# Optimization experiments

Hardware: AMD Instinct MI355X
Metric: run time of the kernel (lower is better)

## Reference

```python
import jax, jax.numpy as jnp
import numpy as np

S_CENTROIDS = 512
RADIUS = 0.5
NSAMPLE = 32
BN_EPS = 1e-5


def farthest_point_sample(xyz, s):
    # xyz: [B, N, 3] -> idx [B, s], deterministic start at index 0
    B, N, _ = xyz.shape

    def step(carry, _):
        dist, far = carry  # dist [B,N], far [B]
        centroid = jnp.take_along_axis(xyz, far[:, None, None], axis=1)  # [B,1,3]
        d = jnp.sum((xyz - centroid) ** 2, axis=-1)  # [B,N]
        dist = jnp.minimum(dist, d)
        nxt = jnp.argmax(dist, axis=-1).astype(jnp.int32)
        return (dist, nxt), far

    init = (jnp.full((B, N), 1e10, dtype=xyz.dtype), jnp.zeros((B,), jnp.int32))
    _, idx = jax.lax.scan(step, init, None, length=s)
    return idx.T  # [B, s]


def query_ball_point(radius, nsample, xyz, new_xyz):
    # xyz [B,N,3], new_xyz [B,S,3] -> group idx [B,S,nsample]
    B, N, _ = xyz.shape
    sqr = jnp.sum((new_xyz[:, :, None, :] - xyz[:, None, :, :]) ** 2, axis=-1)  # [B,S,N]
    gidx = jnp.where(sqr > radius * radius, N, jnp.arange(N, dtype=jnp.int32)[None, None, :])
    gidx = jnp.sort(gidx, axis=-1)[:, :, :nsample]  # closest-index-first valid ids
    first = gidx[:, :, :1]
    gidx = jnp.where(gidx == N, first, gidx)  # pad misses with first neighbor
    return gidx


def bn_relu(h, gamma, beta):
    # training-mode BatchNorm1d over (batch, length) dims of [BS, C, k]
    m = jnp.mean(h, axis=(0, 2), keepdims=True)
    v = jnp.var(h, axis=(0, 2), keepdims=True)
    hn = (h - m) / jnp.sqrt(v + BN_EPS)
    return jax.nn.relu(hn * gamma[None, :, None] + beta[None, :, None])


def setup_inputs() -> dict:
    key = jax.random.key(0)
    k1, k2, k3, k4 = jax.random.split(key, 4)
    B, N, Din, Dout = 16, 2048, 64, 128  # in_channels=2*Din=128
    x = jax.random.normal(k1, (B, Din, N), dtype=jnp.float32)
    coords = jax.random.uniform(k2, (B, N, 3), dtype=jnp.float32, minval=-1.0, maxval=1.0)
    W1 = jax.random.normal(k3, (Dout, 2 * Din), dtype=jnp.float32) * 0.05  # conv1 1x1 kernel
    W2 = jax.random.normal(k4, (Dout, Dout), dtype=jnp.float32) * 0.05    # conv2 1x1 kernel
    gamma1 = jnp.ones((Dout,), jnp.float32); beta1 = jnp.zeros((Dout,), jnp.float32)
    gamma2 = jnp.ones((Dout,), jnp.float32); beta2 = jnp.zeros((Dout,), jnp.float32)
    return {"x": x, "coords": coords, "W1": W1, "W2": W2,
            "gamma1": gamma1, "beta1": beta1, "gamma2": gamma2, "beta2": beta2}


def reference(x, coords, W1, W2, gamma1, beta1, gamma2, beta2):
    B = x.shape[0]
    feats = jnp.transpose(x, (0, 2, 1))  # [B, N, D]

    fidx = farthest_point_sample(coords, S_CENTROIDS)  # [B, s]
    bidx = jnp.arange(B)[:, None]
    new_xyz = coords[bidx, fidx]        # [B, s, 3]
    new_feat = feats[bidx, fidx]        # [B, s, D]

    gidx = query_ball_point(RADIUS, NSAMPLE, coords, new_xyz)  # [B, s, k]
    grouped = feats[jnp.arange(B)[:, None, None], gidx]        # [B, s, k, D]

    center = new_feat[:, :, None, :]
    agg = jnp.concatenate([grouped - center,
                           jnp.broadcast_to(center, grouped.shape)], axis=-1)  # [B, s, k, 2D]

    b, s, k, d = agg.shape
    h = jnp.transpose(agg, (0, 1, 3, 2)).reshape(b * s, d, k)  # [BS, 2D, k]
    h = bn_relu(jnp.einsum('bck,oc->bok', h, W1), gamma1, beta1)
    h = bn_relu(jnp.einsum('bck,oc->bok', h, W2), gamma2, beta2)
    pooled = jnp.max(h, axis=-1)                  # [BS, out]
    new_feature = jnp.transpose(pooled.reshape(b, s, -1), (0, 2, 1))  # [B, out, s]
    return new_xyz, new_feature
```

## Files before the change

kernel.cpp:

```cpp
#include <hip/hip_runtime.h>
#include <cstdint>

typedef unsigned int uint;
typedef unsigned short ushort_t;
typedef unsigned long long ull;
typedef __attribute__((ext_vector_type(8))) short bf16x8;
typedef __attribute__((ext_vector_type(4))) float f32x4;
typedef __attribute__((ext_vector_type(2))) float f32x2;

#define B_   16
#define N_   2048
#define S_   512
#define G_   8192
#define DIN  64
#define DOUT 128
#define K_   32
#define ATS  136

__device__ __forceinline__ uint bf16b(float f) {
  uint u = __float_as_uint(f);
  return (u + 0x7fffu + ((u >> 16) & 1u)) >> 16;
}
__device__ __forceinline__ float bf2f(uint b) { return __uint_as_float(b << 16); }

template<int CTRL, int RM>
__device__ __forceinline__ ull dpp_max_step(ull x) {
  uint lo = (uint)x, hi = (uint)(x >> 32);
  uint nlo = (uint)__builtin_amdgcn_update_dpp((int)lo, (int)lo, CTRL, RM, 0xf, true);
  uint nhi = (uint)__builtin_amdgcn_update_dpp((int)hi, (int)hi, CTRL, RM, 0xf, true);
  ull y = ((ull)nhi << 32) | (ull)nlo;
  return x > y ? x : y;
}

__global__ __launch_bounds__(256) void front_kernel(const float* __restrict__ coords,
    const float* __restrict__ x, const float* __restrict__ W1,
    const float* __restrict__ W2, int* __restrict__ fidx,
    float* __restrict__ out_xyz, ushort_t* __restrict__ xT,
    ushort_t* __restrict__ Bp1, ushort_t* __restrict__ Bpd,
    ushort_t* __restrict__ Bp2) {
  int blk = blockIdx.x;
  int tid = threadIdx.x;
  if (blk < 16) {
    int b = blk;
    const float* cb = coords + (size_t)b * (N_ * 3);
    __shared__ float sptx[N_], spty[N_], sptz[N_];
    __shared__ ull   skey[2][4];
    __shared__ int   sfar[S_];
    int lane = tid & 63, wid = tid >> 6;
    for (int j = tid; j < N_; j += 256) {
      sptx[j] = cb[3 * j]; spty[j] = cb[3 * j + 1]; sptz[j] = cb[3 * j + 2];
    }
    f32x2 px[4], py[4], pz[4], dist[4];
    uint nidx[8];
    int j0 = tid * 8;
#pragma unroll
    for (int p = 0; p < 4; ++p) {
      int j = j0 + 2 * p;
      px[p].x = cb[3 * j];     py[p].x = cb[3 * j + 1]; pz[p].x = cb[3 * j + 2];
      px[p].y = cb[3 * j + 3]; py[p].y = cb[3 * j + 4]; pz[p].y = cb[3 * j + 5];
      dist[p].x = 1e10f; dist[p].y = 1e10f;
      nidx[2 * p] = ~(uint)j; nidx[2 * p + 1] = ~(uint)(j + 1);
    }
    float cx = cb[0], cy = cb[1], cz = cb[2];
    uint far = 0;
    __syncthreads();
    for (int s = 0; s < S_; ++s) {
      if (tid == 0) sfar[s] = (int)far;
      f32x2 c2x = {cx, cx}, c2y = {cy, cy}, c2z = {cz, cz};
      ull best = 0;
#pragma unroll
      for (int p = 0; p < 4; ++p) {
        f32x2 dx, dy, dz, qx, qy, qz, s1, s2;
        asm("v_pk_add_f32 %0, %1, %2 neg_lo:[0,1] neg_hi:[0,1]" : "=v"(dx) : "v"(px[p]), "v"(c2x));
        asm("v_pk_add_f32 %0, %1, %2 neg_lo:[0,1] neg_hi:[0,1]" : "=v"(dy) : "v"(py[p]), "v"(c2y));
        asm("v_pk_add_f32 %0, %1, %2 neg_lo:[0,1] neg_hi:[0,1]" : "=v"(dz) : "v"(pz[p]), "v"(c2z));
        asm("v_pk_mul_f32 %0, %1, %1" : "=v"(qx) : "v"(dx));
        asm("v_pk_mul_f32 %0, %1, %1" : "=v"(qy) : "v"(dy));
        asm("v_pk_mul_f32 %0, %1, %1" : "=v"(qz) : "v"(dz));
        asm("v_pk_add_f32 %0, %1, %2" : "=v"(s1) : "v"(qx), "v"(qy));
        asm("v_pk_add_f32 %0, %1, %2" : "=v"(s2) : "v"(s1), "v"(qz));
        float n0 = fminf(dist[p].x, s2.x);
        float n1 = fminf(dist[p].y, s2.y);
        dist[p].x = n0; dist[p].y = n1;
        ull p0 = ((ull)__float_as_uint(n0) << 32) | (ull)nidx[2 * p];
        ull p1 = ((ull)__float_as_uint(n1) << 32) | (ull)nidx[2 * p + 1];
        best = best > p0 ? best : p0;
        best = best > p1 ? best : p1;
      }
      best = dpp_max_step<0x111, 0xf>(best);
      best = dpp_max_step<0x112, 0xf>(best);
      best = dpp_max_step<0x114, 0xf>(best);
      best = dpp_max_step<0x118, 0xf>(best);
      best = dpp_max_step<0x142, 0xa>(best);
      best = dpp_max_step<0x143, 0xc>(best);
      int pb = s & 1;
      if (lane == 63) skey[pb][wid] = best;
      __syncthreads();
      ull k0 = skey[pb][0], k1 = skey[pb][1], k2 = skey[pb][2], k3 = skey[pb][3];
      uint w0 = ~(uint)k0, w1 = ~(uint)k1, w2 = ~(uint)k2, w3 = ~(uint)k3;
      float x0 = sptx[w0], y0 = spty[w0], z0 = sptz[w0];
      float x1 = sptx[w1], y1 = spty[w1], z1 = sptz[w1];
      float x2 = sptx[w2], y2 = spty[w2], z2 = sptz[w2];
      float x3 = sptx[w3], y3 = spty[w3], z3 = sptz[w3];
      bool t01 = k0 > k1, t23 = k2 > k3;
      ull ka = t01 ? k0 : k1;  float xa = t01 ? x0 : x1, ya = t01 ? y0 : y1, za = t01 ? z0 : z1;
      ull kb = t23 ? k2 : k3;  float xb = t23 ? x2 : x3, yb = t23 ? y2 : y3, zb = t23 ? z2 : z3;
      bool tw = ka > kb;
      far = ~(uint)(tw ? ka : kb);
      cx = tw ? xa : xb; cy = tw ? ya : yb; cz = tw ? za : zb;
    }
    __syncthreads();
    for (int s2 = tid; s2 < S_; s2 += 256) {
      int f = sfar[s2];
      fidx[b * S_ + s2] = f;
      int o = (b * S_ + s2) * 3;
      out_xyz[o] = sptx[f]; out_xyz[o + 1] = spty[f]; out_xyz[o + 2] = sptz[f];
    }
  } else if (blk < 528) {
    __shared__ float tile[64][65];
    int blk2 = blk - 16;
    int b = blk2 >> 5;
    int n0 = (blk2 & 31) * 64;
    int nn = tid & 63, c4 = tid >> 6;
    const float* xb = x + (size_t)b * (DIN * N_);
#pragma unroll
    for (int i = 0; i < 16; ++i) {
      int c = c4 * 16 + i;
      tile[nn][c] = xb[(size_t)c * N_ + n0 + nn];
    }
    __syncthreads();
#pragma unroll
    for (int i = 0; i < 16; ++i) {
      int n = c4 * 16 + i;
      xT[((size_t)b * N_ + n0 + n) * 64 + nn] = (ushort_t)bf16b(tile[n][nn]);
    }
  } else {
    int i = (blk - 528) * 256 + tid;
    int j2 = i & 7, l = (i >> 3) & 63;
    {
      int kc = (i >> 9) & 3, nt = i >> 11;
      int o2 = nt * 16 + (l & 15);
      int c2 = kc * 32 + ((l >> 4) * 8) + j2;
      Bp2[i] = (ushort_t)bf16b(W2[o2 * 128 + c2]);
    }
    if (i < 8192) {
      int kc = (i >> 9) & 1, nt = (i >> 10) & 7;
      int o2 = nt * 16 + (l & 15);
      int c2 = kc * 32 + ((l >> 4) * 8) + j2;
      float wa = W1[o2 * 128 + c2];
      float wb = W1[o2 * 128 + 64 + c2];
      Bp1[i] = (ushort_t)bf16b(wa);
      Bpd[i] = (ushort_t)bf16b(wb - wa);
    }
  }
}

__global__ __launch_bounds__(256) void gemm1_kernel(const ushort_t* __restrict__ xT,
    const float* __restrict__ coords, const int* __restrict__ fidx,
    const ushort_t* __restrict__ Bp1, const ushort_t* __restrict__ Bpd,
    int* __restrict__ gidx, float* __restrict__ psum, float* __restrict__ psq) {
  __shared__ int sgidx[4][K_];
  int tid = threadIdx.x;
  int lane = tid & 63, wid = tid >> 6;
  int g = __builtin_amdgcn_readfirstlane(blockIdx.x * 4 + wid);
  int b = g >> 9;
  const float* cb = coords + (size_t)b * (N_ * 3);
  int nf = fidx[g];
  {
    float cx = cb[3 * nf], cy = cb[3 * nf + 1], cz = cb[3 * nf + 2];
    int cnt = 0, first = 0;
    bool hasfirst = false;
    for (int base = 0; base < N_; base += 64) {
      int j = base + lane;
      float dx = __fsub_rn(cb[3 * j], cx);
      float dy = __fsub_rn(cb[3 * j + 1], cy);
      float dz = __fsub_rn(cb[3 * j + 2], cz);
      float d = __fadd_rn(__fadd_rn(__fmul_rn(dx, dx), __fmul_rn(dy, dy)), __fmul_rn(dz, dz));
      bool in = (d <= 0.25f);
      ull m = __ballot(in);
      if (in) {
        int pos = cnt + __popcll(m & ((1ull << lane) - 1ull));
        if (pos < K_) sgidx[wid][pos] = j;
      }
      if (!hasfirst && m) { first = base + (__ffsll((long long)m) - 1); hasfirst = true; }
      cnt += __popcll(m);
      if (cnt >= K_) break;
    }
    if (cnt < K_) {
      for (int p = cnt + lane; p < K_; p += 64) sgidx[wid][p] = first;
    }
  }
  if (lane < K_) gidx[g * K_ + lane] = sgidx[wid][lane];
  int l15 = lane & 15, r8 = (lane >> 4) * 8;
  const ushort_t* xb64 = xT + (size_t)b * N_ * 64;
  f32x4 acc[2][8];
#pragma unroll
  for (int nt = 0; nt < 8; ++nt) acc[0][nt] = (f32x4){0.f, 0.f, 0.f, 0.f};
#pragma unroll
  for (int kc = 0; kc < 2; ++kc) {
    bf16x8 cu = *(const bf16x8*)(xb64 + nf * 64 + kc * 32 + r8);
#pragma unroll
    for (int nt = 0; nt < 8; ++nt) {
      bf16x8 bf = *(const bf16x8*)(Bpd + ((nt * 2 + kc) * 64 + lane) * 8);
      acc[0][nt] = __builtin_amdgcn_mfma_f32_16x16x32_bf16(cu, bf, acc[0][nt], 0, 0, 0);
    }
  }
#pragma unroll
  for (int nt = 0; nt < 8; ++nt) acc[1][nt] = acc[0][nt];
  int gi0 = sgidx[wid][l15];
  int gi1 = sgidx[wid][16 + l15];
#pragma unroll
  for (int kc = 0; kc < 2; ++kc) {
    bf16x8 af0 = *(const bf16x8*)(xb64 + (size_t)gi0 * 64 + kc * 32 + r8);
    bf16x8 af1 = *(const bf16x8*)(xb64 + (size_t)gi1 * 64 + kc * 32 + r8);
#pragma unroll
    for (int nt = 0; nt < 8; ++nt) {
      bf16x8 bf = *(const bf16x8*)(Bp1 + ((nt * 2 + kc) * 64 + lane) * 8);
      acc[0][nt] = __builtin_amdgcn_mfma_f32_16x16x32_bf16(af0, bf, acc[0][nt], 0, 0, 0);
      acc[1][nt] = __builtin_amdgcn_mfma_f32_16x16x32_bf16(af1, bf, acc[1][nt], 0, 0, 0);
    }
  }
#pragma unroll
  for (int nt = 0; nt < 8; ++nt) {
    float s = 0.f, q = 0.f;
#pragma unroll
    for (int mt = 0; mt < 2; ++mt)
#pragma unroll
      for (int r = 0; r < 4; ++r) { float a = acc[mt][nt][r]; s += a; q = fmaf(a, a, q); }
    s += __shfl_xor(s, 16, 64); s += __shfl_xor(s, 32, 64);
    q += __shfl_xor(q, 16, 64); q += __shfl_xor(q, 32, 64);
    if (lane < 16) {
      int o = nt * 16 + lane;
      psum[o * G_ + g] = s; psq[o * G_ + g] = q;
    }
  }
}

__global__ __launch_bounds__(256) void bn_finalize(const float* __restrict__ psum,
    const float* __restrict__ psq, const float* __restrict__ gamma,
    const float* __restrict__ beta, float* __restrict__ bnp) {
  int o = blockIdx.x, tid = threadIdx.x;
  double s = 0.0, q = 0.0;
  for (int g = tid; g < G_; g += 256) { s += (double)psum[o * G_ + g]; q += (double)psq[o * G_ + g]; }
  __shared__ double ss[256], qq[256];
  ss[tid] = s; qq[tid] = q; __syncthreads();
  for (int off = 128; off > 0; off >>= 1) {
    if (tid < off) { ss[tid] += ss[tid + off]; qq[tid] += qq[tid + off]; }
    __syncthreads();
  }
  if (tid == 0) {
    double n = 262144.0;
    double mean = ss[0] / n, var = qq[0] / n - mean * mean;
    float scv = (float)((double)gamma[o] / sqrt(var + 1e-5));
    bnp[2 * o] = scv;
    bnp[2 * o + 1] = (float)((double)beta[o] - mean * (double)scv);
  }
}

__global__ __launch_bounds__(256) void gemm2_kernel(const ushort_t* __restrict__ xT,
    const int* __restrict__ fidx, const int* __restrict__ gidx,
    const ushort_t* __restrict__ Bp1, const ushort_t* __restrict__ Bpd,
    const ushort_t* __restrict__ Bp2, const float* __restrict__ bnp1,
    float* __restrict__ psum, float* __restrict__ psq,
    float* __restrict__ hmax, float* __restrict__ hmin) {
  __shared__ ushort_t actT[4][32 * ATS];
  int tid = threadIdx.x;
  int lane = tid & 63, wid = tid >> 6;
  int g = __builtin_amdgcn_readfirstlane(blockIdx.x * 4 + wid);
  int b = g >> 9;
  int l15 = lane & 15, r8 = (lane >> 4) * 8;
  const ushort_t* xb64 = xT + (size_t)b * N_ * 64;
  int nf = fidx[g];
  f32x4 acc[2][8];
#pragma unroll
  for (int nt = 0; nt < 8; ++nt) acc[0][nt] = (f32x4){0.f, 0.f, 0.f, 0.f};
#pragma unroll
  for (int kc = 0; kc < 2; ++kc) {
    bf16x8 cu = *(const bf16x8*)(xb64 + nf * 64 + kc * 32 + r8);
#pragma unroll
    for (int nt = 0; nt < 8; ++nt) {
      bf16x8 bf = *(const bf16x8*)(Bpd + ((nt * 2 + kc) * 64 + lane) * 8);
      acc[0][nt] = __builtin_amdgcn_mfma_f32_16x16x32_bf16(cu, bf, acc[0][nt], 0, 0, 0);
    }
  }
#pragma unroll
  for (int nt = 0; nt < 8; ++nt) acc[1][nt] = acc[0][nt];
  int gi0 = gidx[g * K_ + l15];
  int gi1 = gidx[g * K_ + 16 + l15];
#pragma unroll
  for (int kc = 0; kc < 2; ++kc) {
    bf16x8 af0 = *(const bf16x8*)(xb64 + (size_t)gi0 * 64 + kc * 32 + r8);
    bf16x8 af1 = *(const bf16x8*)(xb64 + (size_t)gi1 * 64 + kc * 32 + r8);
#pragma unroll
    for (int nt = 0; nt < 8; ++nt) {
      bf16x8 bf = *(const bf16x8*)(Bp1 + ((nt * 2 + kc) * 64 + lane) * 8);
      acc[0][nt] = __builtin_amdgcn_mfma_f32_16x16x32_bf16(af0, bf, acc[0][nt], 0, 0, 0);
      acc[1][nt] = __builtin_amdgcn_mfma_f32_16x16x32_bf16(af1, bf, acc[1][nt], 0, 0, 0);
    }
  }
  float s1v[8], t1v[8];
#pragma unroll
  for (int nt = 0; nt < 8; ++nt) {
    int o = nt * 16 + l15;
    s1v[nt] = bnp1[2 * o]; t1v[nt] = bnp1[2 * o + 1];
  }
  ushort_t* aw = actT[wid];
#pragma unroll
  for (int mt = 0; mt < 2; ++mt)
#pragma unroll
    for (int r = 0; r < 4; ++r) {
      int k = mt * 16 + (lane >> 4) * 4 + r;
#pragma unroll
      for (int nt = 0; nt < 8; ++nt) {
        float a = fmaxf(fmaf(acc[mt][nt][r], s1v[nt], t1v[nt]), 0.f);
        aw[k * ATS + nt * 16 + l15] = (ushort_t)bf16b(a);
      }
    }
  f32x4 acc2[2][8];
#pragma unroll
  for (int mt = 0; mt < 2; ++mt)
#pragma unroll
    for (int nt = 0; nt < 8; ++nt) acc2[mt][nt] = (f32x4){0.f, 0.f, 0.f, 0.f};
#pragma unroll
  for (int kc = 0; kc < 4; ++kc) {
    bf16x8 afrag[2];
#pragma unroll
    for (int mt = 0; mt < 2; ++mt)
      afrag[mt] = *(const bf16x8*)(aw + (mt * 16 + l15) * ATS + kc * 32 + r8);
#pragma unroll
    for (int nt = 0; nt < 8; ++nt) {
      bf16x8 bfrag = *(const bf16x8*)(Bp2 + ((nt * 4 + kc) * 64 + lane) * 8);
      acc2[0][nt] = __builtin_amdgcn_mfma_f32_16x16x32_bf16(afrag[0], bfrag, acc2[0][nt], 0, 0, 0);
      acc2[1][nt] = __builtin_amdgcn_mfma_f32_16x16x32_bf16(afrag[1], bfrag, acc2[1][nt], 0, 0, 0);
    }
  }
#pragma unroll
  for (int nt = 0; nt < 8; ++nt) {
    float s = 0.f, q = 0.f, mx = -1e30f, mn = 1e30f;
#pragma unroll
    for (int mt = 0; mt < 2; ++mt)
#pragma unroll
      for (int r = 0; r < 4; ++r) {
        float a = acc2[mt][nt][r];
        s += a; q = fmaf(a, a, q); mx = fmaxf(mx, a); mn = fminf(mn, a);
      }
    s += __shfl_xor(s, 16, 64); s += __shfl_xor(s, 32, 64);
    q += __shfl_xor(q, 16, 64); q += __shfl_xor(q, 32, 64);
    mx = fmaxf(mx, __shfl_xor(mx, 16, 64)); mx = fmaxf(mx, __shfl_xor(mx, 32, 64));
    mn = fminf(mn, __shfl_xor(mn, 16, 64)); mn = fminf(mn, __shfl_xor(mn, 32, 64));
    if (lane < 16) {
      int o = nt * 16 + lane;
      psum[o * G_ + g] = s; psq[o * G_ + g] = q;
      hmax[o * G_ + g] = mx; hmin[o * G_ + g] = mn;
    }
  }
}

__global__ __launch_bounds__(256) void bn2pool_kernel(const float* __restrict__ psum,
    const float* __restrict__ psq, const float* __restrict__ gamma,
    const float* __restrict__ beta, const float* __restrict__ hmax,
    const float* __restrict__ hmin, float* __restrict__ out) {
  int o = blockIdx.x, tid = threadIdx.x;
  double s = 0.0, q = 0.0;
  for (int g = tid; g < G_; g += 256) { s += (double)psum[o * G_ + g]; q += (double)psq[o * G_ + g]; }
  __shared__ double ss[256], qq[256];
  __shared__ float sb[2];
  ss[tid] = s; qq[tid] = q; __syncthreads();
  for (int off = 128; off > 0; off >>= 1) {
    if (tid < off) { ss[tid] += ss[tid + off]; qq[tid] += qq[tid + off]; }
    __syncthreads();
  }
  if (tid == 0) {
    double n = 262144.0;
    double mean = ss[0] / n, var = qq[0] / n - mean * mean;
    float scv = (float)((double)gamma[o] / sqrt(var + 1e-5));
    sb[0] = scv;
    sb[1] = (float)((double)beta[o] - mean * (double)scv);
  }
  __syncthreads();
  float scv = sb[0], tf = sb[1];
  for (int g = tid; g < G_; g += 256) {
    float v = (scv >= 0.f) ? hmax[o * G_ + g] : hmin[o * G_ + g];
    int b = g >> 9, s2 = g & 511;
    out[((b << 7) + o) * 512 + s2] = fmaxf(fmaf(scv, v, tf), 0.f);
  }
}

extern "C" void kernel_launch(void* const* d_in, const int* in_sizes, int n_in,
                              void* d_out, int out_size, void* d_ws, size_t ws_size,
                              hipStream_t stream) {
  const float* x      = (const float*)d_in[0];
  const float* coords = (const float*)d_in[1];
  const float* W1     = (const float*)d_in[2];
  const float* W2     = (const float*)d_in[3];
  const float* gamma1 = (const float*)d_in[4];
  const float* beta1  = (const float*)d_in[5];
  const float* gamma2 = (const float*)d_in[6];
  const float* beta2  = (const float*)d_in[7];
  float* out = (float*)d_out;
  char* ws = (char*)d_ws;
  float* psum1 = (float*)(ws);
  float* psq1  = (float*)(ws + 4194304);
  float* psum2 = (float*)(ws + 8388608);
  float* psq2  = (float*)(ws + 12582912);
  float* hmax  = (float*)(ws + 16777216);
  float* hmin  = (float*)(ws + 20971520);
  ushort_t* xT = (ushort_t*)(ws + 25165824);
  ushort_t* Bp1 = (ushort_t*)(ws + 29360128);
  ushort_t* Bpd = (ushort_t*)(ws + 29376512);
  ushort_t* Bp2 = (ushort_t*)(ws + 29392896);
  float* bnp1  = (float*)(ws + 29425664);
  int* fidx    = (int*)(ws + 29427712);
  int* gidx    = (int*)(ws + 29460480);

  front_kernel<<<592, 256, 0, stream>>>(coords, x, W1, W2, fidx, out, xT, Bp1, Bpd, Bp2);
  gemm1_kernel<<<2048, 256, 0, stream>>>(xT, coords, fidx, Bp1, Bpd, gidx, psum1, psq1);
  bn_finalize<<<128, 256, 0, stream>>>(psum1, psq1, gamma1, beta1, bnp1);
  gemm2_kernel<<<2048, 256, 0, stream>>>(xT, fidx, gidx, Bp1, Bpd, Bp2, bnp1,
                                         psum2, psq2, hmax, hmin);
  bn2pool_kernel<<<128, 256, 0, stream>>>(psum2, psq2, gamma2, beta2, hmax, hmin,
                                          out + 24576);
}
```

Baseline: 350.5 us.

## Run farthest-point sampling in a single wavefront per batch without block barriers

Farthest-point sampling becomes its own kernel with one 64-lane wavefront per batch. Each lane holds 32 points in registers and tracks its local argmax with a float value plus a small index, instead of packing 64-bit keys per point. Each step's result comes from a DPP reduction and a readlane, which removes the per-iteration LDS key exchange and __syncthreads. The x transpose and weight packing move to a separate aux kernel. That adds a launch, and the aux work now runs after FPS instead of overlapping with it in the same grid.

Result: slower. 557.7 us (+59.1%).

```diff
diff --git a/kernel.cpp b/kernel.cpp
--- a/kernel.cpp
+++ b/kernel.cpp
@@ -32,95 +32,81 @@
   return x > y ? x : y;
 }
 
-__global__ __launch_bounds__(256) void front_kernel(const float* __restrict__ coords,
-    const float* __restrict__ x, const float* __restrict__ W1,
-    const float* __restrict__ W2, int* __restrict__ fidx,
-    float* __restrict__ out_xyz, ushort_t* __restrict__ xT,
-    ushort_t* __restrict__ Bp1, ushort_t* __restrict__ Bpd,
-    ushort_t* __restrict__ Bp2) {
+__global__ __launch_bounds__(64, 1) void fps1_kernel(const float* __restrict__ coords,
+                                                     int* __restrict__ fidx,
+                                                     float* __restrict__ out_xyz) {
+  int b = blockIdx.x;
+  int lane = threadIdx.x;
+  const float* cb = coords + (size_t)b * (N_ * 3);
+  __shared__ float sptx[N_], spty[N_], sptz[N_];
+  __shared__ int sfar[S_];
+  f32x2 px[16], py[16], pz[16], dist[16];
+  const float* lb = cb + lane * 96;
+#pragma unroll
+  for (int i = 0; i < 16; ++i) {
+    float4 v4 = *(const float4*)(lb + 6 * i);
+    float2 v2 = *(const float2*)(lb + 6 * i + 4);
+    px[i] = (f32x2){v4.x, v4.w};
+    py[i] = (f32x2){v4.y, v2.x};
+    pz[i] = (f32x2){v4.z, v2.y};
+    dist[i] = (f32x2){1e10f, 1e10f};
+    *(f32x2*)&sptx[lane * 32 + 2 * i] = px[i];
+    *(f32x2*)&spty[lane * 32 + 2 * i] = py[i];
+    *(f32x2*)&sptz[lane * 32 + 2 * i] = pz[i];
+  }
+  float cx = cb[0], cy = cb[1], cz = cb[2];
+  uint far = 0;
+  uint jbase = (uint)lane * 32;
+  for (int s = 0; s < S_; ++s) {
+    if (lane == 0) sfar[s] = (int)far;
+    f32x2 c2x = {cx, cx}, c2y = {cy, cy}, c2z = {cz, cz};
+    float bestv = -1.f; uint bestloc = 0;
+#pragma unroll
+    for (int i = 0; i < 16; ++i) {
+      f32x2 dx, dy, dz, qx, qy, qz, s1, s2;
+      asm("v_pk_add_f32 %0, %1, %2 neg_lo:[0,1] neg_hi:[0,1]" : "=v"(dx) : "v"(px[i]), "v"(c2x));
+      asm("v_pk_add_f32 %0, %1, %2 neg_lo:[0,1] neg_hi:[0,1]" : "=v"(dy) : "v"(py[i]), "v"(c2y));
+      asm("v_pk_add_f32 %0, %1, %2 neg_lo:[0,1] neg_hi:[0,1]" : "=v"(dz) : "v"(pz[i]), "v"(c2z));
+      asm("v_pk_mul_f32 %0, %1, %1" : "=v"(qx) : "v"(dx));
+      asm("v_pk_mul_f32 %0, %1, %1" : "=v"(qy) : "v"(dy));
+      asm("v_pk_mul_f32 %0, %1, %1" : "=v"(qz) : "v"(dz));
+      asm("v_pk_add_f32 %0, %1, %2" : "=v"(s1) : "v"(qx), "v"(qy));
+      asm("v_pk_add_f32 %0, %1, %2" : "=v"(s2) : "v"(s1), "v"(qz));
+      float n0 = fminf(dist[i].x, s2.x);
+      float n1 = fminf(dist[i].y, s2.y);
+      dist[i].x = n0; dist[i].y = n1;
+      bool g0 = n0 > bestv; bestv = g0 ? n0 : bestv; bestloc = g0 ? (uint)(2 * i) : bestloc;
+      bool g1 = n1 > bestv; bestv = g1 ? n1 : bestv; bestloc = g1 ? (uint)(2 * i + 1) : bestloc;
+    }
+    ull best = ((ull)__float_as_uint(bestv) << 32) | (ull)(~(jbase + bestloc));
+    best = dpp_max_step<0x111, 0xf>(best);
+    best = dpp_max_step<0x112, 0xf>(best);
+    best = dpp_max_step<0x114, 0xf>(best);
+    best = dpp_max_step<0x118, 0xf>(best);
+    best = dpp_max_step<0x142, 0xa>(best);
+    best = dpp_max_step<0x143, 0xc>(best);
+    uint klo = (uint)__builtin_amdgcn_readlane((int)(uint)best, 63);
+    far = ~klo;
+    cx = sptx[far]; cy = spty[far]; cz = sptz[far];
+  }
+  for (int s2 = lane; s2 < S_; s2 += 64) {
+    int f = sfar[s2];
+    fidx[b * S_ + s2] = f;
+    int o = (b * S_ + s2) * 3;
+    out_xyz[o] = sptx[f]; out_xyz[o + 1] = spty[f]; out_xyz[o + 2] = sptz[f];
+  }
+}
+
+__global__ __launch_bounds__(256) void aux_kernel(const float* __restrict__ x,
+    const float* __restrict__ W1, const float* __restrict__ W2,
+    ushort_t* __restrict__ xT, ushort_t* __restrict__ Bp1,
+    ushort_t* __restrict__ Bpd, ushort_t* __restrict__ Bp2) {
   int blk = blockIdx.x;
   int tid = threadIdx.x;
-  if (blk < 16) {
-    int b = blk;
-    const float* cb = coords + (size_t)b * (N_ * 3);
-    __shared__ float sptx[N_], spty[N_], sptz[N_];
-    __shared__ ull   skey[2][4];
-    __shared__ int   sfar[S_];
-    int lane = tid & 63, wid = tid >> 6;
-    for (int j = tid; j < N_; j += 256) {
-      sptx[j] = cb[3 * j]; spty[j] = cb[3 * j + 1]; sptz[j] = cb[3 * j + 2];
-    }
-    f32x2 px[4], py[4], pz[4], dist[4];
-    uint nidx[8];
-    int j0 = tid * 8;
-#pragma unroll
-    for (int p = 0; p < 4; ++p) {
-      int j = j0 + 2 * p;
-      px[p].x = cb[3 * j];     py[p].x = cb[3 * j + 1]; pz[p].x = cb[3 * j + 2];
-      px[p].y = cb[3 * j + 3]; py[p].y = cb[3 * j + 4]; pz[p].y = cb[3 * j + 5];
-      dist[p].x = 1e10f; dist[p].y = 1e10f;
-      nidx[2 * p] = ~(uint)j; nidx[2 * p + 1] = ~(uint)(j + 1);
-    }
-    float cx = cb[0], cy = cb[1], cz = cb[2];
-    uint far = 0;
-    __syncthreads();
-    for (int s = 0; s < S_; ++s) {
-      if (tid == 0) sfar[s] = (int)far;
-      f32x2 c2x = {cx, cx}, c2y = {cy, cy}, c2z = {cz, cz};
-      ull best = 0;
-#pragma unroll
-      for (int p = 0; p < 4; ++p) {
-        f32x2 dx, dy, dz, qx, qy, qz, s1, s2;
-        asm("v_pk_add_f32 %0, %1, %2 neg_lo:[0,1] neg_hi:[0,1]" : "=v"(dx) : "v"(px[p]), "v"(c2x));
-        asm("v_pk_add_f32 %0, %1, %2 neg_lo:[0,1] neg_hi:[0,1]" : "=v"(dy) : "v"(py[p]), "v"(c2y));
-        asm("v_pk_add_f32 %0, %1, %2 neg_lo:[0,1] neg_hi:[0,1]" : "=v"(dz) : "v"(pz[p]), "v"(c2z));
-        asm("v_pk_mul_f32 %0, %1, %1" : "=v"(qx) : "v"(dx));
-        asm("v_pk_mul_f32 %0, %1, %1" : "=v"(qy) : "v"(dy));
-        asm("v_pk_mul_f32 %0, %1, %1" : "=v"(qz) : "v"(dz));
-        asm("v_pk_add_f32 %0, %1, %2" : "=v"(s1) : "v"(qx), "v"(qy));
-        asm("v_pk_add_f32 %0, %1, %2" : "=v"(s2) : "v"(s1), "v"(qz));
-        float n0 = fminf(dist[p].x, s2.x);
-        float n1 = fminf(dist[p].y, s2.y);
-        dist[p].x = n0; dist[p].y = n1;
-        ull p0 = ((ull)__float_as_uint(n0) << 32) | (ull)nidx[2 * p];
-        ull p1 = ((ull)__float_as_uint(n1) << 32) | (ull)nidx[2 * p + 1];
-        best = best > p0 ? best : p0;
-        best = best > p1 ? best : p1;
-      }
-      best = dpp_max_step<0x111, 0xf>(best);
-      best = dpp_max_step<0x112, 0xf>(best);
-      best = dpp_max_step<0x114, 0xf>(best);
-      best = dpp_max_step<0x118, 0xf>(best);
-      best = dpp_max_step<0x142, 0xa>(best);
-      best = dpp_max_step<0x143, 0xc>(best);
-      int pb = s & 1;
-      if (lane == 63) skey[pb][wid] = best;
-      __syncthreads();
-      ull k0 = skey[pb][0], k1 = skey[pb][1], k2 = skey[pb][2], k3 = skey[pb][3];
-      uint w0 = ~(uint)k0, w1 = ~(uint)k1, w2 = ~(uint)k2, w3 = ~(uint)k3;
-      float x0 = sptx[w0], y0 = spty[w0], z0 = sptz[w0];
-      float x1 = sptx[w1], y1 = spty[w1], z1 = sptz[w1];
-      float x2 = sptx[w2], y2 = spty[w2], z2 = sptz[w2];
-      float x3 = sptx[w3], y3 = spty[w3], z3 = sptz[w3];
-      bool t01 = k0 > k1, t23 = k2 > k3;
-      ull ka = t01 ? k0 : k1;  float xa = t01 ? x0 : x1, ya = t01 ? y0 : y1, za = t01 ? z0 : z1;
-      ull kb = t23 ? k2 : k3;  float xb = t23 ? x2 : x3, yb = t23 ? y2 : y3, zb = t23 ? z2 : z3;
-      bool tw = ka > kb;
-      far = ~(uint)(tw ? ka : kb);
-      cx = tw ? xa : xb; cy = tw ? ya : yb; cz = tw ? za : zb;
-    }
-    __syncthreads();
-    for (int s2 = tid; s2 < S_; s2 += 256) {
-      int f = sfar[s2];
-      fidx[b * S_ + s2] = f;
-      int o = (b * S_ + s2) * 3;
-      out_xyz[o] = sptx[f]; out_xyz[o + 1] = spty[f]; out_xyz[o + 2] = sptz[f];
-    }
-  } else if (blk < 528) {
+  if (blk < 512) {
     __shared__ float tile[64][65];
-    int blk2 = blk - 16;
-    int b = blk2 >> 5;
-    int n0 = (blk2 & 31) * 64;
+    int b = blk >> 5;
+    int n0 = (blk & 31) * 64;
     int nn = tid & 63, c4 = tid >> 6;
     const float* xb = x + (size_t)b * (DIN * N_);
 #pragma unroll
@@ -135,7 +121,7 @@
       xT[((size_t)b * N_ + n0 + n) * 64 + nn] = (ushort_t)bf16b(tile[n][nn]);
     }
   } else {
-    int i = (blk - 528) * 256 + tid;
+    int i = (blk - 512) * 256 + tid;
     int j2 = i & 7, l = (i >> 3) & 63;
     {
       int kc = (i >> 9) & 3, nt = i >> 11;
@@ -413,7 +399,8 @@
   int* fidx    = (int*)(ws + 29427712);
   int* gidx    = (int*)(ws + 29460480);
 
-  front_kernel<<<592, 256, 0, stream>>>(coords, x, W1, W2, fidx, out, xT, Bp1, Bpd, Bp2);
+  fps1_kernel<<<16, 64, 0, stream>>>(coords, fidx, out);
+  aux_kernel<<<576, 256, 0, stream>>>(x, W1, W2, xT, Bp1, Bpd, Bp2);
   gemm1_kernel<<<2048, 256, 0, stream>>>(xT, coords, fidx, Bp1, Bpd, gidx, psum1, psq1);
   bn_finalize<<<128, 256, 0, stream>>>(psum1, psq1, gamma1, beta1, bnp1);
   gemm2_kernel<<<2048, 256, 0, stream>>>(xT, fidx, gidx, Bp1, Bpd, Bp2, bnp1,
```

## Transpose BN partial-stat layout and split reductions into two-stage kernels

Applied to the files above, without the earlier changes.

The per-group partial sums, squares, max and min are now stored group-major ([G][128]) instead of channel-major. The GEMM epilogue stores become contiguous across the 16 lanes. The BN statistics reduction is split into a 128-block partial pass and a single-block finalize, replacing the per-channel block reductions. Pooling becomes its own kernel that transposes through shared memory for coalesced output writes. This adds two extra kernel launches and a dependency on a single-block kernel.

New measurement: 363.8 us. +3.8%, slower.

```diff
diff --git a/kernel.cpp b/kernel.cpp
--- a/kernel.cpp
+++ b/kernel.cpp
@@ -231,29 +231,51 @@
     q += __shfl_xor(q, 16, 64); q += __shfl_xor(q, 32, 64);
     if (lane < 16) {
       int o = nt * 16 + lane;
-      psum[o * G_ + g] = s; psq[o * G_ + g] = q;
-    }
-  }
-}
-
-__global__ __launch_bounds__(256) void bn_finalize(const float* __restrict__ psum,
-    const float* __restrict__ psq, const float* __restrict__ gamma,
+      psum[(size_t)g * 128 + o] = s; psq[(size_t)g * 128 + o] = q;
+    }
+  }
+}
+
+__global__ __launch_bounds__(256) void bnA_kernel(const float* __restrict__ psum,
+    const float* __restrict__ psq, double* __restrict__ part_s,
+    double* __restrict__ part_q) {
+  int bid = blockIdx.x, tid = threadIdx.x;
+  int o = tid & 127, half = tid >> 7;
+  int g0 = bid * 64;
+  double s = 0.0, q = 0.0;
+  for (int r = half; r < 64; r += 2) {
+    s += (double)psum[(size_t)(g0 + r) * 128 + o];
+    q += (double)psq[(size_t)(g0 + r) * 128 + o];
+  }
+  __shared__ double ds[256], dq[256];
+  ds[tid] = s; dq[tid] = q;
+  __syncthreads();
+  if (tid < 128) {
+    part_s[bid * 128 + tid] = ds[tid] + ds[tid + 128];
+    part_q[bid * 128 + tid] = dq[tid] + dq[tid + 128];
+  }
+}
+
+__global__ __launch_bounds__(256) void bnB_kernel(const double* __restrict__ part_s,
+    const double* __restrict__ part_q, const float* __restrict__ gamma,
     const float* __restrict__ beta, float* __restrict__ bnp) {
-  int o = blockIdx.x, tid = threadIdx.x;
+  int tid = threadIdx.x;
+  int o = tid & 127, half = tid >> 7;
   double s = 0.0, q = 0.0;
-  for (int g = tid; g < G_; g += 256) { s += (double)psum[o * G_ + g]; q += (double)psq[o * G_ + g]; }
-  __shared__ double ss[256], qq[256];
-  ss[tid] = s; qq[tid] = q; __syncthreads();
-  for (int off = 128; off > 0; off >>= 1) {
-    if (tid < off) { ss[tid] += ss[tid + off]; qq[tid] += qq[tid + off]; }
-    __syncthreads();
-  }
-  if (tid == 0) {
+  for (int p = half; p < 128; p += 2) {
+    s += part_s[p * 128 + o];
+    q += part_q[p * 128 + o];
+  }
+  __shared__ double ds[256], dq[256];
+  ds[tid] = s; dq[tid] = q;
+  __syncthreads();
+  if (tid < 128) {
+    double S = ds[tid] + ds[tid + 128], Q = dq[tid] + dq[tid + 128];
     double n = 262144.0;
-    double mean = ss[0] / n, var = qq[0] / n - mean * mean;
-    float scv = (float)((double)gamma[o] / sqrt(var + 1e-5));
-    bnp[2 * o] = scv;
-    bnp[2 * o + 1] = (float)((double)beta[o] - mean * (double)scv);
+    double mean = S / n, var = Q / n - mean * mean;
+    float scv = (float)((double)gamma[tid] / sqrt(var + 1e-5));
+    bnp[2 * tid] = scv;
+    bnp[2 * tid + 1] = (float)((double)beta[tid] - mean * (double)scv);
   }
 }
 
@@ -350,39 +372,35 @@
     mn = fminf(mn, __shfl_xor(mn, 16, 64)); mn = fminf(mn, __shfl_xor(mn, 32, 64));
     if (lane < 16) {
       int o = nt * 16 + lane;
-      psum[o * G_ + g] = s; psq[o * G_ + g] = q;
-      hmax[o * G_ + g] = mx; hmin[o * G_ + g] = mn;
-    }
-  }
-}
-
-__global__ __launch_bounds__(256) void bn2pool_kernel(const float* __restrict__ psum,
-    const float* __restrict__ psq, const float* __restrict__ gamma,
-    const float* __restrict__ beta, const float* __restrict__ hmax,
-    const float* __restrict__ hmin, float* __restrict__ out) {
-  int o = blockIdx.x, tid = threadIdx.x;
-  double s = 0.0, q = 0.0;
-  for (int g = tid; g < G_; g += 256) { s += (double)psum[o * G_ + g]; q += (double)psq[o * G_ + g]; }
-  __shared__ double ss[256], qq[256];
-  __shared__ float sb[2];
-  ss[tid] = s; qq[tid] = q; __syncthreads();
-  for (int off = 128; off > 0; off >>= 1) {
-    if (tid < off) { ss[tid] += ss[tid + off]; qq[tid] += qq[tid + off]; }
-    __syncthreads();
-  }
-  if (tid == 0) {
-    double n = 262144.0;
-    double mean = ss[0] / n, var = qq[0] / n - mean * mean;
-    float scv = (float)((double)gamma[o] / sqrt(var + 1e-5));
-    sb[0] = scv;
-    sb[1] = (float)((double)beta[o] - mean * (double)scv);
+      psum[(size_t)g * 128 + o] = s; psq[(size_t)g * 128 + o] = q;
+      hmax[(size_t)g * 128 + o] = mx; hmin[(size_t)g * 128 + o] = mn;
+    }
+  }
+}
+
+__global__ __launch_bounds__(256) void pool_kernel(const float* __restrict__ hmax,
+    const float* __restrict__ hmin, const float* __restrict__ bnp2,
+    float* __restrict__ out) {
+  __shared__ float hx[16][132], hn[16][132];
+  int bid = blockIdx.x;
+  int g0 = bid * 16;
+  int b = g0 >> 9, s0 = g0 & 511;
+  int tid = threadIdx.x;
+  int col = tid & 127, rp = tid >> 7;
+#pragma unroll
+  for (int j = 0; j < 8; ++j) {
+    int row = j * 2 + rp;
+    hx[row][col] = hmax[(size_t)(g0 + row) * 128 + col];
+    hn[row][col] = hmin[(size_t)(g0 + row) * 128 + col];
   }
   __syncthreads();
-  float scv = sb[0], tf = sb[1];
-  for (int g = tid; g < G_; g += 256) {
-    float v = (scv >= 0.f) ? hmax[o * G_ + g] : hmin[o * G_ + g];
-    int b = g >> 9, s2 = g & 511;
-    out[((b << 7) + o) * 512 + s2] = fmaxf(fmaf(scv, v, tf), 0.f);
+  int o = tid >> 1, sh = (tid & 1) * 8;
+  float scv = bnp2[2 * o], tf = bnp2[2 * o + 1];
+  float* op = out + ((size_t)(b * 128 + o) * 512) + s0 + sh;
+#pragma unroll
+  for (int j = 0; j < 8; ++j) {
+    float v = (scv >= 0.f) ? hx[sh + j][o] : hn[sh + j][o];
+    op[j] = fmaxf(fmaf(scv, v, tf), 0.f);
   }
 }
 
@@ -410,14 +428,19 @@
   ushort_t* Bpd = (ushort_t*)(ws + 29376512);
   ushort_t* Bp2 = (ushort_t*)(ws + 29392896);
   float* bnp1  = (float*)(ws + 29425664);
+  float* bnp2  = (float*)(ws + 29426688);
   int* fidx    = (int*)(ws + 29427712);
   int* gidx    = (int*)(ws + 29460480);
+  double* part_s = (double*)(ws + 30509056);
+  double* part_q = (double*)(ws + 30640128);
 
   front_kernel<<<592, 256, 0, stream>>>(coords, x, W1, W2, fidx, out, xT, Bp1, Bpd, Bp2);
   gemm1_kernel<<<2048, 256, 0, stream>>>(xT, coords, fidx, Bp1, Bpd, gidx, psum1, psq1);
-  bn_finalize<<<128, 256, 0, stream>>>(psum1, psq1, gamma1, beta1, bnp1);
+  bnA_kernel<<<128, 256, 0, stream>>>(psum1, psq1, part_s, part_q);
+  bnB_kernel<<<1, 256, 0, stream>>>(part_s, part_q, gamma1, beta1, bnp1);
   gemm2_kernel<<<2048, 256, 0, stream>>>(xT, fidx, gidx, Bp1, Bpd, Bp2, bnp1,
                                          psum2, psq2, hmax, hmin);
-  bn2pool_kernel<<<128, 256, 0, stream>>>(psum2, psq2, gamma2, beta2, hmax, hmin,
-                                          out + 24576);
-}
+  bnA_kernel<<<128, 256, 0, stream>>>(psum2, psq2, part_s, part_q);
+  bnB_kernel<<<1, 256, 0, stream>>>(part_s, part_q, gamma2, beta2, bnp2);
+  pool_kernel<<<512, 256, 0, stream>>>(hmax, hmin, bnp2, out + 24576);
+}
```
